# Optimization experiments

Measured on AMD Instinct MI355X. Metric: run time of the kernel, lower is better.

The kernel has to match this reference:

```python
import jax, jax.numpy as jnp
import numpy as np

D_MODEL = 1024
NUM_HEADS = 16
DEPTH = D_MODEL // NUM_HEADS  # 64
BATCH, SEQ = 4, 2048


def setup_inputs() -> dict:
    key = jax.random.key(0)
    ks = jax.random.split(key, 9)
    s = 1.0 / np.sqrt(D_MODEL)
    x = jax.random.normal(ks[0], (BATCH, SEQ, D_MODEL), dtype=jnp.float32)
    # Per-head Dense weights stacked on a leading head axis [H, d_model, depth]
    Wq = jax.random.normal(ks[1], (NUM_HEADS, D_MODEL, DEPTH), dtype=jnp.float32) * s
    Wk = jax.random.normal(ks[2], (NUM_HEADS, D_MODEL, DEPTH), dtype=jnp.float32) * s
    Wv = jax.random.normal(ks[3], (NUM_HEADS, D_MODEL, DEPTH), dtype=jnp.float32) * s
    bq = jnp.zeros((NUM_HEADS, DEPTH), dtype=jnp.float32)
    bk = jnp.zeros((NUM_HEADS, DEPTH), dtype=jnp.float32)
    bv = jnp.zeros((NUM_HEADS, DEPTH), dtype=jnp.float32)
    Wo = jax.random.normal(ks[4], (D_MODEL, D_MODEL), dtype=jnp.float32) * s
    bo = jnp.zeros((D_MODEL,), dtype=jnp.float32)
    return {"x": x, "Wq": Wq, "bq": bq, "Wk": Wk, "bk": bk,
            "Wv": Wv, "bv": bv, "Wo": Wo, "bo": bo}


def reference(x, Wq, bq, Wk, bk, Wv, bv, Wo, bo):
    # Batched equivalent of the per-head loop: project, attend, concat heads.
    q = jnp.einsum('bsd,hde->bhse', x, Wq) + bq[:, None, :]  # [B,H,S,depth]
    k = jnp.einsum('bsd,hde->bhse', x, Wk) + bk[:, None, :]
    v = jnp.einsum('bsd,hde->bhse', x, Wv) + bv[:, None, :]
    scale = 1.0 / jnp.sqrt(jnp.asarray(DEPTH, dtype=x.dtype))
    scores = jnp.einsum('bhse,bhte->bhst', q, k) * scale      # [B,H,S,S]
    weights = jax.nn.softmax(scores, axis=-1)
    heads = jnp.einsum('bhst,bhte->bhse', weights, v)         # [B,H,S,depth]
    # concat head outputs along last axis in head order (tf.concat axis=-1)
    multi = jnp.transpose(heads, (0, 2, 1, 3)).reshape(x.shape[0], x.shape[1], D_MODEL)
    return multi @ Wo + bo
```

## Files before the change

### kernel.cpp

```cpp
#include <hip/hip_runtime.h>
#include <hip/hip_bf16.h>

#define BATCH 4
#define SEQ   2048
#define DM    1024
#define NH    16
#define DEPTH 64
#define ROWS  (BATCH*SEQ)
#define NQKV  (3*DM)
#define BH    (BATCH*NH)

typedef __attribute__((ext_vector_type(8))) short bf16x8;
typedef __attribute__((ext_vector_type(4))) float f32x4;
typedef __attribute__((ext_vector_type(16))) float f32x16;
typedef unsigned short u16;
typedef unsigned int   u32;

__device__ __forceinline__ u16 f2bf(float f) {
    union { float f; unsigned u; } v; v.f = f;
    unsigned r = v.u + 0x7fff + ((v.u >> 16) & 1);
    return (u16)(r >> 16);
}

__device__ __forceinline__ u32 pk2bf(float a, float b) {
#if __has_builtin(__builtin_amdgcn_cvt_pk_bf16_f32)
    typedef __attribute__((ext_vector_type(2))) __bf16 v2bf;
    union { v2bf v; u32 u; } u_;
    u_.v = __builtin_amdgcn_cvt_pk_bf16_f32(a, b);
    return u_.u;
#else
    return (u32)f2bf(a) | ((u32)f2bf(b) << 16);
#endif
}

__device__ __forceinline__ void g2l16(void* lds, const void* g) {
    __builtin_amdgcn_global_load_lds((const __attribute__((address_space(1))) void*)g,
                                     (__attribute__((address_space(3))) void*)lds, 16, 0, 0);
}

__device__ __forceinline__ bf16x8 frag8(const u16* tile, int row, int gl) {
    return *(const bf16x8*)(tile + row * 64 + ((gl ^ (row & 7)) * 8));
}

__device__ __forceinline__ f32x16 mfma32(bf16x8 a, bf16x8 b, f32x16 c) {
    return __builtin_amdgcn_mfma_f32_32x32x16_bf16(a, b, c, 0, 0, 0);
}

__global__ __launch_bounds__(256) void k_prep(const float* __restrict__ x,
                                              const float* __restrict__ Wq, const float* __restrict__ Wk,
                                              const float* __restrict__ Wv, const float* __restrict__ Wo,
                                              u16* __restrict__ xb, u16* __restrict__ BT, u16* __restrict__ WoT) {
    __shared__ u16 T[64][65];
    int tid = threadIdx.x;
    int bx = blockIdx.x;
    if (bx < 2048) {
        int i = bx * 4096 + tid * 4;
        for (int l = 0; l < 4; ++l) {
            float4 v = *(const float4*)(x + i + l * 1024);
            ushort4 o; o.x = f2bf(v.x); o.y = f2bf(v.y); o.z = f2bf(v.z); o.w = f2bf(v.w);
            *(ushort4*)(xb + i + l * 1024) = o;
        }
        return;
    }
    if (bx < 2816) {
        int q = bx - 2048;
        int kt = q & 15, mh = q >> 4, m = mh >> 4, h = mh & 15;
        const float* W = (m == 0) ? Wq : (m == 1) ? Wk : Wv;
        const float* src = W + ((size_t)h * 1024 + kt * 64) * 64;
        int e = tid & 63, r0 = tid >> 6;
        for (int i = 0; i < 16; ++i) { int r = i * 4 + r0; T[r][e] = f2bf(src[r * 64 + e]); }
        __syncthreads();
        int kk = tid & 63, e0 = tid >> 6;
        u16* dst = BT + ((size_t)m * 1024 + h * 64) * 1024 + kt * 64;
        for (int i = 0; i < 16; ++i) { int ee = i * 4 + e0; dst[ee * 1024 + kk] = T[kk][ee]; }
        return;
    }
    {
        int q = bx - 2816;
        int kt = q & 15, nt = q >> 4;
        const float* src = Wo + (size_t)kt * 64 * 1024 + nt * 64;
        int c = tid & 63, r0 = tid >> 6;
        for (int i = 0; i < 16; ++i) { int r = i * 4 + r0; T[r][c] = f2bf(src[r * 1024 + c]); }
        __syncthreads();
        int kk = tid & 63, e0 = tid >> 6;
        u16* dst = WoT + (size_t)nt * 64 * 1024 + kt * 64;
        for (int i = 0; i < 16; ++i) { int ee = i * 4 + e0; dst[ee * 1024 + kk] = T[kk][ee]; }
    }
}

__global__ __launch_bounds__(256) void k_gemm_qkv(const u16* __restrict__ xb, const u16* __restrict__ Wt,
                                                  const float* __restrict__ bq, const float* __restrict__ bk,
                                                  const float* __restrict__ bv,
                                                  u16* __restrict__ Q, u16* __restrict__ K, u16* __restrict__ VT) {
    __shared__ u16 Al[128 * 64];
    __shared__ u16 Bl[128 * 64];
    int tid = threadIdx.x;
    int wave = tid >> 6, lane = tid & 63, ln = lane & 15, quad = lane >> 4;
    int b = blockIdx.x;
    bool isvt = (b >= 1024);
    int row0, col0;
    const u16 *Am, *Bm;
    if (!isvt) {
        col0 = (b & 15) * 128; row0 = (b >> 4) * 128;
        Am = xb + (size_t)row0 * 1024; Bm = Wt + (size_t)col0 * 1024;
    } else {
        int b2 = b - 1024;
        col0 = (b2 & 63) * 128; row0 = (b2 >> 6) * 128;
        Am = Wt + (size_t)2048 * 1024 + (size_t)row0 * 1024; Bm = xb + (size_t)col0 * 1024;
    }
    int moff = (wave >> 1) * 64, noff = (wave & 1) * 64;
    f32x4 acc[4][4] = {};

    for (int k0 = 0; k0 < 1024; k0 += 64) {
        for (int l = 0; l < 4; ++l) {
            int idx = tid + l * 256, r = idx >> 3, gs = ((idx & 7) ^ (r & 7)) * 8;
            g2l16(&Al[idx * 8], Am + r * 1024 + k0 + gs);
            g2l16(&Bl[idx * 8], Bm + r * 1024 + k0 + gs);
        }
        __syncthreads();
        for (int kk = 0; kk < 2; ++kk) {
            bf16x8 a[4], bb[4];
            for (int i = 0; i < 4; ++i) a[i]  = frag8(Al, moff + i * 16 + ln, kk * 4 + quad);
            for (int j = 0; j < 4; ++j) bb[j] = frag8(Bl, noff + j * 16 + ln, kk * 4 + quad);
            for (int i = 0; i < 4; ++i)
                for (int j = 0; j < 4; ++j)
                    acc[i][j] = __builtin_amdgcn_mfma_f32_16x16x32_bf16(a[i], bb[j], acc[i][j], 0, 0, 0);
        }
        __syncthreads();
    }

    if (!isvt) {
        const float QSCALE = 0.125f * 1.4426950408889634f;
        for (int j = 0; j < 4; ++j) {
            int c = col0 + noff + j * 16 + ln;
            int m = c >> 10, h = (c >> 6) & 15, e = c & 63;
            const float* bias = (m == 0) ? bq : bk;
            float bval = bias[h * 64 + e];
            for (int i = 0; i < 4; ++i)
                for (int r = 0; r < 4; ++r) {
                    int rowg = row0 + moff + i * 16 + quad * 4 + r;
                    int b_ = rowg >> 11, s = rowg & 2047;
                    int bh = b_ * 16 + h;
                    float v = acc[i][j][r] + bval;
                    if (m == 0) Q[(bh * 2048 + s) * 64 + e] = f2bf(v * QSCALE);
                    else        K[(bh * 2048 + s) * 64 + e] = f2bf(v);
                }
        }
    } else {
        for (int j = 0; j < 4; ++j) {
            int c = col0 + noff + j * 16 + ln;
            int b_ = c >> 11, s = c & 2047;
            for (int i = 0; i < 4; ++i)
                for (int r = 0; r < 4; ++r) {
                    int ii = row0 + moff + i * 16 + quad * 4 + r;
                    float v = acc[i][j][r] + bv[ii];
                    VT[((size_t)b_ * 1024 + ii) * 2048 + s] = f2bf(v);
                }
        }
    }
}

__global__ __launch_bounds__(128, 2) void k_attn(const u16* __restrict__ Q, const u16* __restrict__ K,
                                                 const u16* __restrict__ VT, u16* __restrict__ A2) {
    __shared__ u16 Ql[128 * 64];
    __shared__ u16 Kl[64 * 64];
    __shared__ u16 Vl[64 * 64];
    __shared__ float linv[128];
    int tid = threadIdx.x;
    int wave = tid >> 6, lane = tid & 63, l31 = lane & 31, h = lane >> 5;
    int bh = blockIdx.y;
    int m0 = blockIdx.x * 128;
    const u16* Qb = Q + (size_t)bh * 2048 * 64;
    const u16* Kb = K + (size_t)bh * 2048 * 64;
    const u16* Vb = VT + (size_t)bh * 64 * 2048;

    const u16* kp[4]; const u16* vp[4]; int dsti[4];
    for (int l = 0; l < 4; ++l) {
        int idx = tid + l * 128, r = idx >> 3, gs = ((idx & 7) ^ (r & 7)) * 8;
        dsti[l] = idx * 8;
        kp[l] = Kb + r * 64 + gs;
        vp[l] = Vb + r * 2048 + gs;
    }
    for (int l = 0; l < 8; ++l) {
        int idx = tid + l * 128, r = idx >> 3, gs = ((idx & 7) ^ (r & 7)) * 8;
        g2l16(&Ql[idx * 8], Qb + (m0 + r) * 64 + gs);
    }
    for (int l = 0; l < 4; ++l) { g2l16(&Kl[dsti[l]], kp[l]); g2l16(&Vl[dsti[l]], vp[l]); }
    __syncthreads();

    bf16x8 qb[2][4];
    for (int qt = 0; qt < 2; ++qt)
        for (int s = 0; s < 4; ++s)
            qb[qt][s] = frag8(Ql, wave * 64 + qt * 32 + l31, 2 * s + h);

    f32x16 oacc[2][2] = {};
    float lsum[2] = {0.f, 0.f};

    for (int t = 0; t < 32; ++t) {
        f32x16 sc[2][2] = {};
        for (int s = 0; s < 4; ++s) {
            bf16x8 kf0 = frag8(Kl, l31,      2 * s + h);
            bf16x8 kf1 = frag8(Kl, 32 + l31, 2 * s + h);
            for (int qt = 0; qt < 2; ++qt) {
                sc[0][qt] = mfma32(kf0, qb[qt][s], sc[0][qt]);
                sc[1][qt] = mfma32(kf1, qb[qt][s], sc[1][qt]);
            }
        }

        for (int qt = 0; qt < 2; ++qt) {
            int prow = wave * 64 + qt * 32 + l31;
            int rm = prow & 7;
            char* pbase = (char*)Ql + prow * 128 + 8 * h;
            float sq = 0.f;
            for (int kt = 0; kt < 2; ++kt)
                for (int g = 0; g < 4; ++g) {
                    float p0 = __builtin_amdgcn_exp2f(sc[kt][qt][g * 4 + 0]);
                    float p1 = __builtin_amdgcn_exp2f(sc[kt][qt][g * 4 + 1]);
                    float p2 = __builtin_amdgcn_exp2f(sc[kt][qt][g * 4 + 2]);
                    float p3 = __builtin_amdgcn_exp2f(sc[kt][qt][g * 4 + 3]);
                    sq += (p0 + p1) + (p2 + p3);
                    uint2 w; w.x = pk2bf(p0, p1); w.y = pk2bf(p2, p3);
                    *(uint2*)(pbase + ((kt * 4 + g) ^ rm) * 16) = w;
                }
            lsum[qt] += sq;
        }

        for (int s = 0; s < 4; ++s) {
            bf16x8 ap0 = frag8(Ql, wave * 64 + l31,      2 * s + h);
            bf16x8 ap1 = frag8(Ql, wave * 64 + 32 + l31, 2 * s + h);
            bf16x8 bv0 = frag8(Vl, l31,      2 * s + h);
            bf16x8 bv1 = frag8(Vl, 32 + l31, 2 * s + h);
            oacc[0][0] = mfma32(ap0, bv0, oacc[0][0]);
            oacc[0][1] = mfma32(ap0, bv1, oacc[0][1]);
            oacc[1][0] = mfma32(ap1, bv0, oacc[1][0]);
            oacc[1][1] = mfma32(ap1, bv1, oacc[1][1]);
        }
        __syncthreads();
        if (t < 31) {
            for (int l = 0; l < 4; ++l) {
                g2l16(&Kl[dsti[l]], kp[l] + (t + 1) * 4096);
                g2l16(&Vl[dsti[l]], vp[l] + (t + 1) * 64);
            }
        }
        __syncthreads();
    }

    for (int qt = 0; qt < 2; ++qt) {
        float l2 = lsum[qt] + __shfl_xor(lsum[qt], 32);
        linv[wave * 64 + qt * 32 + l31] = 1.0f / l2;
    }
    int b_ = bh >> 4, hh = bh & 15;
    for (int qt = 0; qt < 2; ++qt)
        for (int g = 0; g < 4; ++g) {
            f32x4 iv = *(f32x4*)&linv[wave * 64 + qt * 32 + 8 * g + 4 * h];
            for (int dt = 0; dt < 2; ++dt)
                for (int r = 0; r < 4; ++r) {
                    int row = b_ * 2048 + m0 + wave * 64 + qt * 32 + 8 * g + 4 * h + r;
                    A2[row * 1024 + hh * 64 + dt * 32 + l31] = f2bf(oacc[qt][dt][g * 4 + r] * iv[r]);
                }
        }
}

__global__ __launch_bounds__(256) void k_gemm_out(const u16* __restrict__ A, const u16* __restrict__ BT,
                                                  const float* __restrict__ bo, float* __restrict__ out) {
    __shared__ u16 Al[128 * 64];
    __shared__ u16 Bl[128 * 64];
    int tid = threadIdx.x;
    int wave = tid >> 6, lane = tid & 63, ln = lane & 15, quad = lane >> 4;
    int row0 = blockIdx.y * 128;
    int col0 = blockIdx.x * 128;
    int moff = (wave >> 1) * 64, noff = (wave & 1) * 64;
    f32x4 acc[4][4] = {};

    for (int k0 = 0; k0 < 1024; k0 += 64) {
        for (int l = 0; l < 4; ++l) {
            int idx = tid + l * 256, r = idx >> 3, gs = ((idx & 7) ^ (r & 7)) * 8;
            g2l16(&Al[idx * 8], A  + (row0 + r) * 1024 + k0 + gs);
            g2l16(&Bl[idx * 8], BT + (col0 + r) * 1024 + k0 + gs);
        }
        __syncthreads();
        for (int kk = 0; kk < 2; ++kk) {
            bf16x8 a[4], b[4];
            for (int i = 0; i < 4; ++i) a[i] = frag8(Al, moff + i * 16 + ln, kk * 4 + quad);
            for (int j = 0; j < 4; ++j) b[j] = frag8(Bl, noff + j * 16 + ln, kk * 4 + quad);
            for (int i = 0; i < 4; ++i)
                for (int j = 0; j < 4; ++j)
                    acc[i][j] = __builtin_amdgcn_mfma_f32_16x16x32_bf16(a[i], b[j], acc[i][j], 0, 0, 0);
        }
        __syncthreads();
    }

    for (int j = 0; j < 4; ++j) {
        int c = col0 + noff + j * 16 + ln;
        float bias = bo[c];
        for (int i = 0; i < 4; ++i)
            for (int r = 0; r < 4; ++r) {
                int rowg = row0 + moff + i * 16 + quad * 4 + r;
                out[rowg * 1024 + c] = acc[i][j][r] + bias;
            }
    }
}

extern "C" void kernel_launch(void* const* d_in, const int* in_sizes, int n_in,
                              void* d_out, int out_size, void* d_ws, size_t ws_size,
                              hipStream_t stream) {
    const float* x  = (const float*)d_in[0];
    const float* Wq = (const float*)d_in[1];
    const float* bq = (const float*)d_in[2];
    const float* Wk = (const float*)d_in[3];
    const float* bk = (const float*)d_in[4];
    const float* Wv = (const float*)d_in[5];
    const float* bv = (const float*)d_in[6];
    const float* Wo = (const float*)d_in[7];
    const float* bo = (const float*)d_in[8];
    float* out = (float*)d_out;

    char* ws = (char*)d_ws;
    u16* xb    = (u16*)ws; ws += (size_t)ROWS * DM * 2;
    u16* WqkvT = (u16*)ws; ws += (size_t)NQKV * DM * 2;
    u16* WoT   = (u16*)ws; ws += (size_t)DM * DM * 2;
    u16* Qb    = (u16*)ws; ws += (size_t)BH * SEQ * DEPTH * 2;
    u16* Kb    = (u16*)ws; ws += (size_t)BH * SEQ * DEPTH * 2;
    u16* VTb   = (u16*)ws; ws += (size_t)BH * SEQ * DEPTH * 2;
    u16* A2    = (u16*)ws; ws += (size_t)ROWS * DM * 2;

    k_prep     <<<dim3(3072),   dim3(256), 0, stream>>>(x, Wq, Wk, Wv, Wo, xb, WqkvT, WoT);
    k_gemm_qkv <<<dim3(1536),   dim3(256), 0, stream>>>(xb, WqkvT, bq, bk, bv, Qb, Kb, VTb);
    k_attn     <<<dim3(16, 64), dim3(128), 0, stream>>>(Qb, Kb, VTb, A2);
    k_gemm_out <<<dim3(8, 64),  dim3(256), 0, stream>>>(A2, WoT, bo, out);
}
```

Before: 288.0 us.

## Keep softmax probabilities in registers via permlane swap and double-buffer V tiles

The attention kernel now feeds the exp'd scores straight into the PV MFMA as A operands, using permlane32 swaps to rearrange the accumulator layout into operand layout. This removes the LDS round-trip for P. Q and K fragments are loaded directly from global memory into registers instead of being staged through LDS. V tiles are double-buffered in LDS with an async prefetch of the next tile, which removes one barrier per iteration. The block grows to 256 threads (256 query rows), trading more register pressure and uncoalesced per-lane global K loads for less LDS traffic and fewer syncs.

```diff
diff --git a/kernel.cpp b/kernel.cpp
--- a/kernel.cpp
+++ b/kernel.cpp
@@ -31,6 +31,27 @@
 #else
     return (u32)f2bf(a) | ((u32)f2bf(b) << 16);
 #endif
+}
+
+__device__ __forceinline__ void pl32swap(u32& x, u32& y) {
+#if __has_builtin(__builtin_amdgcn_permlane32_swap)
+    typedef __attribute__((ext_vector_type(2))) int v2i;
+    v2i r = __builtin_amdgcn_permlane32_swap((int)x, (int)y, false, false);
+    x = (u32)r[0]; y = (u32)r[1];
+#else
+    u32 sx = (u32)__shfl_xor((int)x, 32);
+    u32 sy = (u32)__shfl_xor((int)y, 32);
+    bool hi = (threadIdx.x & 32) != 0;
+    u32 nx = hi ? sy : x;
+    u32 ny = hi ? y : sx;
+    x = nx; y = ny;
+#endif
+}
+
+__device__ __forceinline__ bf16x8 pack4(u32 a, u32 b, u32 c, u32 d) {
+    union { u32 u[4]; bf16x8 v; } x;
+    x.u[0] = a; x.u[1] = b; x.u[2] = c; x.u[3] = d;
+    return x.v;
 }
 
 __device__ __forceinline__ void g2l16(void* lds, const void* g) {
@@ -160,86 +181,76 @@
     }
 }
 
-__global__ __launch_bounds__(128, 2) void k_attn(const u16* __restrict__ Q, const u16* __restrict__ K,
+__global__ __launch_bounds__(256, 2) void k_attn(const u16* __restrict__ Q, const u16* __restrict__ K,
                                                  const u16* __restrict__ VT, u16* __restrict__ A2) {
-    __shared__ u16 Ql[128 * 64];
-    __shared__ u16 Kl[64 * 64];
-    __shared__ u16 Vl[64 * 64];
-    __shared__ float linv[128];
+    __shared__ u16 Vl[2][64 * 64];
+    __shared__ float linv[256];
     int tid = threadIdx.x;
-    int wave = tid >> 6, lane = tid & 63, l31 = lane & 31, h = lane >> 5;
+    int w = tid >> 6, lane = tid & 63, l31 = lane & 31, h = lane >> 5;
     int bh = blockIdx.y;
-    int m0 = blockIdx.x * 128;
+    int m0 = blockIdx.x * 256;
     const u16* Qb = Q + (size_t)bh * 2048 * 64;
     const u16* Kb = K + (size_t)bh * 2048 * 64;
     const u16* Vb = VT + (size_t)bh * 64 * 2048;
 
-    const u16* kp[4]; const u16* vp[4]; int dsti[4];
-    for (int l = 0; l < 4; ++l) {
-        int idx = tid + l * 128, r = idx >> 3, gs = ((idx & 7) ^ (r & 7)) * 8;
-        dsti[l] = idx * 8;
-        kp[l] = Kb + r * 64 + gs;
-        vp[l] = Vb + r * 2048 + gs;
-    }
-    for (int l = 0; l < 8; ++l) {
-        int idx = tid + l * 128, r = idx >> 3, gs = ((idx & 7) ^ (r & 7)) * 8;
-        g2l16(&Ql[idx * 8], Qb + (m0 + r) * 64 + gs);
-    }
-    for (int l = 0; l < 4; ++l) { g2l16(&Kl[dsti[l]], kp[l]); g2l16(&Vl[dsti[l]], vp[l]); }
-    __syncthreads();
+    int sidx[2]; const u16* vsrc[2];
+    for (int rr = 0; rr < 2; ++rr) {
+        int idx = tid + rr * 256, r = idx >> 3, g = (idx & 7) ^ (r & 7);
+        sidx[rr] = idx * 8;
+        vsrc[rr] = Vb + r * 2048 + g * 8;
+    }
+    g2l16(&Vl[0][sidx[0]], vsrc[0]);
+    g2l16(&Vl[0][sidx[1]], vsrc[1]);
 
     bf16x8 qb[2][4];
     for (int qt = 0; qt < 2; ++qt)
         for (int s = 0; s < 4; ++s)
-            qb[qt][s] = frag8(Ql, wave * 64 + qt * 32 + l31, 2 * s + h);
+            qb[qt][s] = *(const bf16x8*)(Qb + (m0 + w * 64 + qt * 32 + l31) * 64 + s * 16 + h * 8);
+    __syncthreads();
 
     f32x16 oacc[2][2] = {};
     float lsum[2] = {0.f, 0.f};
 
     for (int t = 0; t < 32; ++t) {
-        f32x16 sc[2][2] = {};
-        for (int s = 0; s < 4; ++s) {
-            bf16x8 kf0 = frag8(Kl, l31,      2 * s + h);
-            bf16x8 kf1 = frag8(Kl, 32 + l31, 2 * s + h);
+        const u16* Kt = Kb + t * 64 * 64;
+        bf16x8 kf[2][4];
+        for (int kt = 0; kt < 2; ++kt)
+            for (int s = 0; s < 4; ++s)
+                kf[kt][s] = *(const bf16x8*)(Kt + (kt * 32 + l31) * 64 + s * 16 + h * 8);
+
+        if (t < 31) {
+            g2l16(&Vl[(t + 1) & 1][sidx[0]], vsrc[0] + (t + 1) * 64);
+            g2l16(&Vl[(t + 1) & 1][sidx[1]], vsrc[1] + (t + 1) * 64);
+        }
+        const u16* vb = Vl[t & 1];
+
+        for (int kt = 0; kt < 2; ++kt) {
+            f32x16 sc[2] = {};
+            for (int s = 0; s < 4; ++s) {
+                sc[0] = mfma32(kf[kt][s], qb[0][s], sc[0]);
+                sc[1] = mfma32(kf[kt][s], qb[1][s], sc[1]);
+            }
+            bf16x8 vf00 = frag8(vb, l31,      kt * 4 + h);
+            bf16x8 vf01 = frag8(vb, l31,      kt * 4 + 2 + h);
+            bf16x8 vf10 = frag8(vb, 32 + l31, kt * 4 + h);
+            bf16x8 vf11 = frag8(vb, 32 + l31, kt * 4 + 2 + h);
             for (int qt = 0; qt < 2; ++qt) {
-                sc[0][qt] = mfma32(kf0, qb[qt][s], sc[0][qt]);
-                sc[1][qt] = mfma32(kf1, qb[qt][s], sc[1][qt]);
-            }
-        }
-
-        for (int qt = 0; qt < 2; ++qt) {
-            int prow = wave * 64 + qt * 32 + l31;
-            int rm = prow & 7;
-            char* pbase = (char*)Ql + prow * 128 + 8 * h;
-            float sq = 0.f;
-            for (int kt = 0; kt < 2; ++kt)
-                for (int g = 0; g < 4; ++g) {
-                    float p0 = __builtin_amdgcn_exp2f(sc[kt][qt][g * 4 + 0]);
-                    float p1 = __builtin_amdgcn_exp2f(sc[kt][qt][g * 4 + 1]);
-                    float p2 = __builtin_amdgcn_exp2f(sc[kt][qt][g * 4 + 2]);
-                    float p3 = __builtin_amdgcn_exp2f(sc[kt][qt][g * 4 + 3]);
-                    sq += (p0 + p1) + (p2 + p3);
-                    uint2 w; w.x = pk2bf(p0, p1); w.y = pk2bf(p2, p3);
-                    *(uint2*)(pbase + ((kt * 4 + g) ^ rm) * 16) = w;
+                u32 g[8]; float sq = 0.f;
+                for (int gi = 0; gi < 8; ++gi) {
+                    float p0 = __builtin_amdgcn_exp2f(sc[qt][2 * gi]);
+                    float p1 = __builtin_amdgcn_exp2f(sc[qt][2 * gi + 1]);
+                    sq += p0 + p1;
+                    g[gi] = pk2bf(p0, p1);
                 }
-            lsum[qt] += sq;
-        }
-
-        for (int s = 0; s < 4; ++s) {
-            bf16x8 ap0 = frag8(Ql, wave * 64 + l31,      2 * s + h);
-            bf16x8 ap1 = frag8(Ql, wave * 64 + 32 + l31, 2 * s + h);
-            bf16x8 bv0 = frag8(Vl, l31,      2 * s + h);
-            bf16x8 bv1 = frag8(Vl, 32 + l31, 2 * s + h);
-            oacc[0][0] = mfma32(ap0, bv0, oacc[0][0]);
-            oacc[0][1] = mfma32(ap0, bv1, oacc[0][1]);
-            oacc[1][0] = mfma32(ap1, bv0, oacc[1][0]);
-            oacc[1][1] = mfma32(ap1, bv1, oacc[1][1]);
-        }
-        __syncthreads();
-        if (t < 31) {
-            for (int l = 0; l < 4; ++l) {
-                g2l16(&Kl[dsti[l]], kp[l] + (t + 1) * 4096);
-                g2l16(&Vl[dsti[l]], vp[l] + (t + 1) * 64);
+                lsum[qt] += sq;
+                pl32swap(g[0], g[2]); pl32swap(g[1], g[3]);
+                pl32swap(g[4], g[6]); pl32swap(g[5], g[7]);
+                bf16x8 a0 = pack4(g[0], g[1], g[2], g[3]);
+                bf16x8 a1 = pack4(g[4], g[5], g[6], g[7]);
+                oacc[qt][0] = mfma32(a0, vf00, oacc[qt][0]);
+                oacc[qt][0] = mfma32(a1, vf01, oacc[qt][0]);
+                oacc[qt][1] = mfma32(a0, vf10, oacc[qt][1]);
+                oacc[qt][1] = mfma32(a1, vf11, oacc[qt][1]);
             }
         }
         __syncthreads();
@@ -247,15 +258,15 @@
 
     for (int qt = 0; qt < 2; ++qt) {
         float l2 = lsum[qt] + __shfl_xor(lsum[qt], 32);
-        linv[wave * 64 + qt * 32 + l31] = 1.0f / l2;
+        linv[w * 64 + qt * 32 + l31] = 1.0f / l2;
     }
     int b_ = bh >> 4, hh = bh & 15;
     for (int qt = 0; qt < 2; ++qt)
         for (int g = 0; g < 4; ++g) {
-            f32x4 iv = *(f32x4*)&linv[wave * 64 + qt * 32 + 8 * g + 4 * h];
+            f32x4 iv = *(f32x4*)&linv[w * 64 + qt * 32 + 8 * g + 4 * h];
             for (int dt = 0; dt < 2; ++dt)
                 for (int r = 0; r < 4; ++r) {
-                    int row = b_ * 2048 + m0 + wave * 64 + qt * 32 + 8 * g + 4 * h + r;
+                    int row = b_ * 2048 + m0 + w * 64 + qt * 32 + 8 * g + 4 * h + r;
                     A2[row * 1024 + hh * 64 + dt * 32 + l31] = f2bf(oacc[qt][dt][g * 4 + r] * iv[r]);
                 }
         }
@@ -326,6 +337,6 @@
 
     k_prep     <<<dim3(3072),   dim3(256), 0, stream>>>(x, Wq, Wk, Wv, Wo, xb, WqkvT, WoT);
     k_gemm_qkv <<<dim3(1536),   dim3(256), 0, stream>>>(xb, WqkvT, bq, bk, bv, Qb, Kb, VTb);
-    k_attn     <<<dim3(16, 64), dim3(128), 0, stream>>>(Qb, Kb, VTb, A2);
+    k_attn     <<<dim3(8, 64),  dim3(256), 0, stream>>>(Qb, Kb, VTb, A2);
     k_gemm_out <<<dim3(8, 64),  dim3(256), 0, stream>>>(A2, WoT, bo, out);
 }
```

Measured after the change: 302.9 us. 5.2% more time.
